# Kernel tuning notes

Hardware: AMD Instinct MI355X
Metric: run time of the kernel (lower is better)

Reference implementation:

```python
import math
import jax, jax.numpy as jnp
import numpy as np

B, S, H = 8, 2048, 1024
NH = 1
DH = H // NH          # head dim == hidden since NH=1 (required by module's math)
DT = 64               # distance_type


def setup_inputs() -> dict:
    key = jax.random.key(0)
    ks = jax.random.split(key, 10)
    hidden_states = jax.random.normal(ks[0], (B, S, H), dtype=jnp.float32)
    attention_mask = jnp.zeros((B, 1, 1, S), dtype=jnp.float32)
    word_word_relation = jax.random.randint(ks[1], (B, S, S), 0, DT, dtype=jnp.int32)
    init = 0.02
    Wq = jax.random.normal(ks[2], (H, H), dtype=jnp.float32) * init
    bq = jnp.zeros((H,), dtype=jnp.float32)
    Wk = jax.random.normal(ks[3], (H, H), dtype=jnp.float32) * init
    bk = jnp.zeros((H,), dtype=jnp.float32)
    Wv = jax.random.normal(ks[4], (H, H), dtype=jnp.float32) * init
    bv = jnp.zeros((H,), dtype=jnp.float32)
    dist_emb = jax.random.normal(ks[5], (DT, H), dtype=jnp.float32) * init
    dist_emb = dist_emb.at[0].set(0.0)  # padding_idx=0
    return {
        "hidden_states": hidden_states,
        "attention_mask": attention_mask,
        "word_word_relation": word_word_relation,
        "Wq": Wq, "bq": bq, "Wk": Wk, "bk": bk, "Wv": Wv, "bv": bv,
        "dist_emb": dist_emb,
    }


def reference(hidden_states, attention_mask, word_word_relation,
              Wq, bq, Wk, bk, Wv, bv, dist_emb):
    b, s, h = hidden_states.shape
    def heads(x):  # [b,s,h] -> [b,nh,s,dh]
        return x.reshape(b, s, NH, DH).transpose(0, 2, 1, 3)
    q = heads(hidden_states @ Wq.T + bq)
    k = heads(hidden_states @ Wk.T + bk)
    v = heads(hidden_states @ Wv.T + bv)

    scores = jnp.einsum('bhqd,bhkd->bhqk', q, k)                 # [b,nh,s,s]
    word_dot_distance = jnp.einsum('bhqd,td->bhqt', q, dist_emb) # [b,nh,s,DT]

    idx = word_word_relation[:, None, :, :]                      # [b,1,s,s]
    bias = jnp.take_along_axis(word_dot_distance, idx, axis=3)
    mask_out = (word_word_relation == 1)[:, None].astype(scores.dtype)
    bias = bias * mask_out

    scores = (scores + bias) / math.sqrt(DH) + attention_mask
    probs = jax.nn.softmax(scores, axis=-1)
    ctx = jnp.einsum('bhqk,bhkd->bhqd', probs, v)
    ctx = ctx.transpose(0, 2, 1, 3).reshape(b, s, h)
    return ctx
```

## Files before the change

### kernel.cpp

```cpp
#include <hip/hip_runtime.h>

typedef unsigned short u16;
typedef __bf16 bf16x8 __attribute__((ext_vector_type(8)));
typedef u16 u16x8 __attribute__((ext_vector_type(8)));
typedef float f32x4 __attribute__((ext_vector_type(4)));

#define S_LEN 2048
#define H_LEN 1024

__device__ __forceinline__ u16 f2b(float f) {
  unsigned u = __float_as_uint(f);
  return (u16)((u + 0x7FFFu + ((u >> 16) & 1u)) >> 16);
}
__device__ __forceinline__ float b2f(u16 h) { return __uint_as_float(((unsigned)h) << 16); }

#define GLOAD16(gp, lp)                                   \
  __builtin_amdgcn_global_load_lds(                       \
      (__attribute__((address_space(1))) void*)(gp),      \
      (__attribute__((address_space(3))) void*)(lp), 16, 0, 0)

#define FENCE() asm volatile("" ::: "memory")
#define PBAR()                           \
  do {                                   \
    FENCE();                             \
    __builtin_amdgcn_s_barrier();        \
    FENCE();                             \
  } while (0)
#define WAIT_LGKM0()                                        \
  do {                                                      \
    asm volatile("s_waitcnt lgkmcnt(0)" ::: "memory");      \
    __builtin_amdgcn_sched_barrier(0);                      \
  } while (0)
#define WAIT_VM(n) asm volatile("s_waitcnt vmcnt(" #n ")" ::: "memory")

__device__ __forceinline__ f32x4 MM(bf16x8 a, bf16x8 b, f32x4 c) {
  return __builtin_amdgcn_mfma_f32_16x16x32_bf16(a, b, c, 0, 0, 0);
}

__global__ __launch_bounds__(256) void prep_kernel(
    const float* __restrict__ X, const float* __restrict__ Wq,
    const float* __restrict__ Wk, const float* __restrict__ Wv,
    const float* __restrict__ bq, const float* __restrict__ bk,
    const float* __restrict__ bv, const float* __restrict__ dist,
    const int* __restrict__ rel,
    u16* __restrict__ Xbf, u16* __restrict__ Wbf, float* __restrict__ b_all,
    u16* __restrict__ de1, unsigned* __restrict__ bits, float* __restrict__ d1) {
  size_t tid = (size_t)blockIdx.x * blockDim.x + threadIdx.x;
  size_t nth = (size_t)gridDim.x * blockDim.x;
  for (size_t i = tid; i < 4194304u; i += nth) {
    float4 v = ((const float4*)X)[i];
    ushort4 o; o.x = f2b(v.x); o.y = f2b(v.y); o.z = f2b(v.z); o.w = f2b(v.w);
    ((ushort4*)Xbf)[i] = o;
  }
  for (size_t i = tid; i < 786432u; i += nth) {
    int which = (int)(i >> 18);
    size_t off = i & 262143u;
    const float4* src = (const float4*)(which == 0 ? Wq : (which == 1 ? Wk : Wv));
    float4 v = src[off];
    ushort4 o; o.x = f2b(v.x); o.y = f2b(v.y); o.z = f2b(v.z); o.w = f2b(v.w);
    ((ushort4*)Wbf)[i] = o;
  }
  const int4* r4 = (const int4*)rel;
  for (size_t wi = tid; wi < 1048576u; wi += nth) {
    const int4* s = r4 + wi * 8;
    unsigned m = 0;
#pragma unroll
    for (int u = 0; u < 8; ++u) {
      int4 v = s[u];
      m |= (unsigned)(v.x == 1) << (u * 4 + 0);
      m |= (unsigned)(v.y == 1) << (u * 4 + 1);
      m |= (unsigned)(v.z == 1) << (u * 4 + 2);
      m |= (unsigned)(v.w == 1) << (u * 4 + 3);
    }
    bits[wi] = m;
  }
  for (size_t i = tid; i < 256u; i += nth) {
    float4 v = ((const float4*)(dist + H_LEN))[i];
    ushort4 o; o.x = f2b(v.x); o.y = f2b(v.y); o.z = f2b(v.z); o.w = f2b(v.w);
    ((ushort4*)de1)[i] = o;
  }
  for (size_t i = tid; i < 3072u; i += nth)
    b_all[i] = (i < 1024) ? bq[i] : (i < 2048 ? bk[i - 1024] : bv[i - 2048]);
  for (size_t i = tid; i < 32768u; i += nth) d1[i] = 0.f;
}

struct GArgs {
  const u16* A; const u16* B;
  long long sA, sB;
  int ldA, ldB, K;
  u16 *Qo, *Ko, *Vo; const float* b_all; const u16* de1; float* d1;
  const unsigned* relbits; const float* mask; u16* P; float* denom;
  float* outp;
};

template <int EPI>
__global__ __launch_bounds__(512, 2) void gemm256(GArgs g) {
  int bx, by, bz;
  {
    const int lin = blockIdx.x;
    if constexpr (EPI == 0) {
      const int wg = (lin & 7) * 96 + (lin >> 3);
      by = wg / 12; bx = wg % 12; bz = 0;
    } else if constexpr (EPI == 1) {
      const int wg = (lin & 7) * 64 + (lin >> 3);
      bz = wg >> 6; by = (wg >> 3) & 7; bx = wg & 7;
    } else {
      const int wg = (lin & 7) * 32 + (lin >> 3);
      bz = wg >> 5; by = (wg >> 2) & 7; bx = wg & 3;
    }
  }
  const u16* Abase = g.A + (size_t)bz * g.sA;
  const u16* Bbase = g.B + (size_t)bz * g.sB;
  const int m0 = by * 256, n0 = bx * 256;

  __shared__ u16 smem[65536];

  const int tid = threadIdx.x;
  const int lane = tid & 63, w = tid >> 6;
  const int wm = w >> 2, wn = w & 3;
  const int l15 = lane & 15, quad = lane >> 4;

  f32x4 acc[8][4];
  const f32x4 zero = {0.f, 0.f, 0.f, 0.f};
#pragma unroll
  for (int a = 0; a < 8; ++a)
#pragma unroll
    for (int b = 0; b < 4; ++b) acc[a][b] = zero;

  const u16* gA[4]; const u16* gB[4]; int qoff[4];
#pragma unroll
  for (int r = 0; r < 4; ++r) {
    const int q = r * 512 + tid;
    const int row = q >> 3, ch = q & 7;
    const int chS = ch ^ (row & 7);
    gA[r] = Abase + (size_t)(m0 + row) * g.ldA + chS * 8;
    gB[r] = Bbase + (size_t)(n0 + row) * g.ldB + chS * 8;
    qoff[r] = q * 8;
  }

  const int NT = g.K >> 6;

  auto stage2 = [&](int tile, int pr) {
    if (tile >= NT) return;
    const int boff2 = (tile & 1) << 15;
    const int kt = tile << 6;
    if (pr < 2) {
      GLOAD16(gA[2 * pr] + kt,     &smem[boff2 + qoff[2 * pr]]);
      GLOAD16(gA[2 * pr + 1] + kt, &smem[boff2 + qoff[2 * pr + 1]]);
    } else {
      const int r = 2 * (pr - 2);
      GLOAD16(gB[r] + kt,     &smem[boff2 + 16384 + qoff[r]]);
      GLOAD16(gB[r + 1] + kt, &smem[boff2 + 16384 + qoff[r + 1]]);
    }
  };

  stage2(0, 0); stage2(0, 1); stage2(0, 2); stage2(0, 3);
  stage2(1, 0);
  if (1 < NT) { WAIT_VM(2); } else { WAIT_VM(0); }
  PBAR();

  bf16x8 af0[4][2], af1[4][2], bf0[2][2], bf1[2][2];

  for (int t = 0; t < NT; ++t) {
    const int boff = (t & 1) << 15;
    const u16* Ab = smem + boff;
    const u16* Bb = smem + boff + 16384;

#pragma unroll
    for (int mt = 0; mt < 4; ++mt) {
      const int row = wm * 128 + mt * 16 + l15;
      const int base = row * 64, rx = row & 7;
      af0[mt][0] = *(const bf16x8*)&Ab[base + ((quad ^ rx) << 3)];
      af0[mt][1] = *(const bf16x8*)&Ab[base + (((quad + 4) ^ rx) << 3)];
    }
#pragma unroll
    for (int nt = 0; nt < 2; ++nt) {
      const int row = wn * 64 + nt * 16 + l15;
      const int base = row * 64, rx = row & 7;
      bf0[nt][0] = *(const bf16x8*)&Bb[base + ((quad ^ rx) << 3)];
      bf0[nt][1] = *(const bf16x8*)&Bb[base + (((quad + 4) ^ rx) << 3)];
    }
    stage2(t + 1, 1);
    asm volatile("s_waitcnt lgkmcnt(8)" ::: "memory");
    PBAR();
    WAIT_LGKM0();
    __builtin_amdgcn_s_setprio(1);
#pragma unroll
    for (int mt = 0; mt < 4; ++mt)
#pragma unroll
      for (int nt = 0; nt < 2; ++nt) {
        acc[mt][nt] = MM(af0[mt][0], bf0[nt][0], acc[mt][nt]);
        acc[mt][nt] = MM(af0[mt][1], bf0[nt][1], acc[mt][nt]);
      }
    __builtin_amdgcn_s_setprio(0);
    PBAR();

#pragma unroll
    for (int nt = 0; nt < 2; ++nt) {
      const int row = wn * 64 + (nt + 2) * 16 + l15;
      const int base = row * 64, rx = row & 7;
      bf1[nt][0] = *(const bf16x8*)&Bb[base + ((quad ^ rx) << 3)];
      bf1[nt][1] = *(const bf16x8*)&Bb[base + (((quad + 4) ^ rx) << 3)];
    }
    stage2(t + 1, 2);
    PBAR();
    WAIT_LGKM0();
    __builtin_amdgcn_s_setprio(1);
#pragma unroll
    for (int mt = 0; mt < 4; ++mt)
#pragma unroll
      for (int nt = 0; nt < 2; ++nt) {
        acc[mt][nt + 2] = MM(af0[mt][0], bf1[nt][0], acc[mt][nt + 2]);
        acc[mt][nt + 2] = MM(af0[mt][1], bf1[nt][1], acc[mt][nt + 2]);
      }
    __builtin_amdgcn_s_setprio(0);
    PBAR();

#pragma unroll
    for (int mt = 0; mt < 4; ++mt) {
      const int row = wm * 128 + (mt + 4) * 16 + l15;
      const int base = row * 64, rx = row & 7;
      af1[mt][0] = *(const bf16x8*)&Ab[base + ((quad ^ rx) << 3)];
      af1[mt][1] = *(const bf16x8*)&Ab[base + (((quad + 4) ^ rx) << 3)];
    }
    stage2(t + 1, 3);
    PBAR();
    WAIT_LGKM0();
    __builtin_amdgcn_s_setprio(1);
#pragma unroll
    for (int mt = 0; mt < 4; ++mt)
#pragma unroll
      for (int nt = 0; nt < 2; ++nt) {
        acc[mt + 4][nt] = MM(af1[mt][0], bf0[nt][0], acc[mt + 4][nt]);
        acc[mt + 4][nt] = MM(af1[mt][1], bf0[nt][1], acc[mt + 4][nt]);
      }
    __builtin_amdgcn_s_setprio(0);
    PBAR();

    stage2(t + 2, 0);
    PBAR();
    WAIT_LGKM0();
    __builtin_amdgcn_s_setprio(1);
#pragma unroll
    for (int mt = 0; mt < 4; ++mt)
#pragma unroll
      for (int nt = 0; nt < 2; ++nt) {
        acc[mt + 4][nt + 2] = MM(af1[mt][0], bf1[nt][0], acc[mt + 4][nt + 2]);
        acc[mt + 4][nt + 2] = MM(af1[mt][1], bf1[nt][1], acc[mt + 4][nt + 2]);
      }
    __builtin_amdgcn_s_setprio(0);
    if (t + 2 < NT) {
      WAIT_VM(2);
    } else if (t + 1 < NT) {
      WAIT_VM(0);
    }
    PBAR();
  }

  const int nbase = n0 + wn * 64;

  if constexpr (EPI == 0) {
    const int which = n0 >> 10;
    const int nl0 = n0 & 1023;
    float bv4[4], dw[4];
#pragma unroll
    for (int nt = 0; nt < 4; ++nt) {
      const int col = wn * 64 + nt * 16 + l15;
      bv4[nt] = g.b_all[n0 + col];
      dw[nt] = (which == 0) ? b2f(g.de1[nl0 + col]) : 0.f;
    }
#pragma unroll
    for (int mt = 0; mt < 8; ++mt)
#pragma unroll
      for (int r = 0; r < 4; ++r) {
        const int row = wm * 128 + mt * 16 + quad * 4 + r;
        float part = 0.f;
#pragma unroll
        for (int nt = 0; nt < 4; ++nt) {
          const float v = acc[mt][nt][r] + bv4[nt];
          part += v * dw[nt];
          const int col = wn * 64 + nt * 16 + l15;
          const int chS = (col >> 3) ^ (row & 31);
          smem[row * 256 + chS * 8 + (col & 7)] = f2b(v);
        }
        if (which == 0) {
          part += __shfl_xor(part, 1);
          part += __shfl_xor(part, 2);
          part += __shfl_xor(part, 4);
          part += __shfl_xor(part, 8);
          if (l15 == 0) atomicAdd(&g.d1[m0 + row], part);
        }
      }
    __syncthreads();
    u16* dstbuf = which == 0 ? g.Qo : (which == 1 ? g.Ko : g.Vo);
#pragma unroll
    for (int p = 0; p < 16; ++p) {
      const int flat = p * 512 + tid;
      const int row = flat >> 5, chunk = flat & 31;
      const int chS = chunk ^ (row & 31);
      u16x8 v = *(const u16x8*)&smem[row * 256 + chS * 8];
      *(u16x8*)(dstbuf + (size_t)(m0 + row) * H_LEN + nl0 + chunk * 8) = v;
    }
  }

  if constexpr (EPI == 1) {
    float mk[4];
#pragma unroll
    for (int nt = 0; nt < 4; ++nt) mk[nt] = g.mask[bz * S_LEN + nbase + nt * 16 + l15];
    const size_t bSS = (size_t)bz * S_LEN * S_LEN;
    const int wbase = (n0 + wn * 64) >> 5;
#pragma unroll
    for (int mt = 0; mt < 8; ++mt)
#pragma unroll
      for (int r = 0; r < 4; ++r) {
        const int row = wm * 128 + mt * 16 + quad * 4 + r;
        const int gi = bz * S_LEN + m0 + row;
        const float d1v = g.d1[gi] * 0.03125f;
        const unsigned w0 = g.relbits[(size_t)gi * 64 + wbase];
        const unsigned w1 = g.relbits[(size_t)gi * 64 + wbase + 1];
        float dsum = 0.f;
#pragma unroll
        for (int nt = 0; nt < 4; ++nt) {
          const unsigned word = (nt & 2) ? w1 : w0;
          const int pos = (nt * 16 + l15) & 31;
          const float bias = ((word >> pos) & 1) ? d1v : 0.f;
          const float logit = acc[mt][nt][r] * 0.03125f + bias + mk[nt];
          const float pv = __expf(logit);
          const u16 pb = f2b(pv);
          dsum += b2f(pb);
          const int col = wn * 64 + nt * 16 + l15;
          const int chS = (col >> 3) ^ (row & 31);
          smem[row * 256 + chS * 8 + (col & 7)] = pb;
        }
        dsum += __shfl_xor(dsum, 1);
        dsum += __shfl_xor(dsum, 2);
        dsum += __shfl_xor(dsum, 4);
        dsum += __shfl_xor(dsum, 8);
        if (l15 == 0) atomicAdd(&g.denom[gi], dsum);
      }
    __syncthreads();
#pragma unroll
    for (int p = 0; p < 16; ++p) {
      const int flat = p * 512 + tid;
      const int row = flat >> 5, chunk = flat & 31;
      const int chS = chunk ^ (row & 31);
      u16x8 v = *(const u16x8*)&smem[row * 256 + chS * 8];
      *(u16x8*)(g.P + bSS + (size_t)(m0 + row) * S_LEN + n0 + chunk * 8) = v;
    }
  }

  if constexpr (EPI == 2) {
    const size_t ob = (size_t)bz * S_LEN * H_LEN;
#pragma unroll
    for (int mt = 0; mt < 8; ++mt)
#pragma unroll
      for (int r = 0; r < 4; ++r) {
        const int row = wm * 128 + mt * 16 + quad * 4 + r;
        const float inv = 1.0f / g.denom[bz * S_LEN + m0 + row];
        const size_t rowo = ob + (size_t)(m0 + row) * H_LEN;
#pragma unroll
        for (int nt = 0; nt < 4; ++nt)
          g.outp[rowo + nbase + nt * 16 + l15] = acc[mt][nt][r] * inv;
      }
  }
}

__global__ __launch_bounds__(256) void transpose_v(const u16* __restrict__ V,
                                                   u16* __restrict__ Vt) {
  const int b = blockIdx.z;
  const int j0 = blockIdx.x * 64;
  const int d0 = blockIdx.y * 64;
  __shared__ u16 t[64][72];
  const int tid = threadIdx.x;
  const int tr = tid >> 4;
  const int tc = (tid & 15) * 4;
#pragma unroll
  for (int p = 0; p < 4; ++p) {
    const int jl = p * 16 + tr;
    const u16* src = V + ((size_t)b * S_LEN + (j0 + jl)) * H_LEN + d0 + tc;
    ushort4 v = *(const ushort4*)src;
    t[jl][tc + 0] = v.x; t[jl][tc + 1] = v.y; t[jl][tc + 2] = v.z; t[jl][tc + 3] = v.w;
  }
  __syncthreads();
#pragma unroll
  for (int p = 0; p < 4; ++p) {
    const int dl = p * 16 + tr;
    ushort4 v;
    v.x = t[tc + 0][dl]; v.y = t[tc + 1][dl]; v.z = t[tc + 2][dl]; v.w = t[tc + 3][dl];
    *(ushort4*)(Vt + ((size_t)b * H_LEN + (d0 + dl)) * S_LEN + j0 + tc) = v;
  }
}

extern "C" void kernel_launch(void* const* d_in, const int* in_sizes, int n_in,
                              void* d_out, int out_size, void* d_ws, size_t ws_size,
                              hipStream_t stream) {
  (void)in_sizes; (void)n_in; (void)out_size; (void)ws_size;
  const float* X    = (const float*)d_in[0];
  const float* mask = (const float*)d_in[1];
  const int*   rel  = (const int*)d_in[2];
  const float* Wq   = (const float*)d_in[3];
  const float* bq   = (const float*)d_in[4];
  const float* Wk   = (const float*)d_in[5];
  const float* bk   = (const float*)d_in[6];
  const float* Wv   = (const float*)d_in[7];
  const float* bv   = (const float*)d_in[8];
  const float* dist = (const float*)d_in[9];
  float* out = (float*)d_out;

  char* p = (char*)d_ws;
  u16* Xbf = (u16*)p;      p += (size_t)16384 * 1024 * 2;
  u16* Wbf = (u16*)p;      p += (size_t)3072 * 1024 * 2;
  float* b_all = (float*)p; p += 3072 * 4;
  u16* de1 = (u16*)p;      p += 4096;
  u16* Qb = (u16*)p;       p += (size_t)16384 * 1024 * 2;
  u16* Kb = (u16*)p;       p += (size_t)16384 * 1024 * 2;
  u16* Vb = (u16*)p;       p += (size_t)16384 * 1024 * 2;
  u16* Vt = (u16*)p;       p += (size_t)16384 * 1024 * 2;
  float* d1 = (float*)p;   p += 16384 * 4;
  float* denom = (float*)p; p += 16384 * 4;
  unsigned* relbits = (unsigned*)p; p += (size_t)1048576 * 4;
  u16* P = (u16*)p;        p += (size_t)8 * 2048 * 2048 * 2;

  prep_kernel<<<1024, 256, 0, stream>>>(X, Wq, Wk, Wv, bq, bk, bv, dist, rel,
                                        Xbf, Wbf, b_all, de1, relbits, d1);

  GArgs g0 = {};
  g0.A = Xbf; g0.B = Wbf; g0.sA = 0; g0.sB = 0;
  g0.ldA = 1024; g0.ldB = 1024; g0.K = 1024;
  g0.Qo = Qb; g0.Ko = Kb; g0.Vo = Vb; g0.b_all = b_all; g0.de1 = de1; g0.d1 = d1;
  gemm256<0><<<dim3(768, 1, 1), dim3(512, 1, 1), 0, stream>>>(g0);

  transpose_v<<<dim3(32, 16, 8), dim3(256, 1, 1), 0, stream>>>(Vb, Vt);

  GArgs g1 = {};
  g1.A = Qb; g1.B = Kb; g1.sA = 2048LL * 1024; g1.sB = 2048LL * 1024;
  g1.ldA = 1024; g1.ldB = 1024; g1.K = 1024;
  g1.relbits = relbits; g1.d1 = d1; g1.mask = mask; g1.P = P; g1.denom = denom;
  gemm256<1><<<dim3(512, 1, 1), dim3(512, 1, 1), 0, stream>>>(g1);

  GArgs g2 = {};
  g2.A = P; g2.B = Vt; g2.sA = 2048LL * 2048; g2.sB = 1024LL * 2048;
  g2.ldA = 2048; g2.ldB = 2048; g2.K = 2048;
  g2.denom = denom; g2.outp = out;
  gemm256<2><<<dim3(256, 1, 1), dim3(512, 1, 1), 0, stream>>>(g2);
}
```

Measured before the change: 594.0 us.

## Fuse V transpose into projection epilogue, restage GEMM loads, coalesce relation bitpacking

The V projection epilogue now writes V already transposed through shared memory, so the separate transpose kernel and the intermediate V buffer are removed. The QKV and QK^T GEMMs switch from staggered partial-tile staging to issuing a full tile's loads two tiles ahead with deeper vmcnt waits. The QK^T block index mapping drops the XCD-swizzled order for a plain linear order. The relation-mask bitpacking now has each thread read one contiguous int4 and assemble 32-bit masks with lane shuffles, giving coalesced loads.

```diff
diff --git a/kernel.cpp b/kernel.cpp
--- a/kernel.cpp
+++ b/kernel.cpp
@@ -47,6 +47,7 @@
     u16* __restrict__ de1, unsigned* __restrict__ bits, float* __restrict__ d1) {
   size_t tid = (size_t)blockIdx.x * blockDim.x + threadIdx.x;
   size_t nth = (size_t)gridDim.x * blockDim.x;
+  const int lane = threadIdx.x & 63;
   for (size_t i = tid; i < 4194304u; i += nth) {
     float4 v = ((const float4*)X)[i];
     ushort4 o; o.x = f2b(v.x); o.y = f2b(v.y); o.z = f2b(v.z); o.w = f2b(v.w);
@@ -61,18 +62,17 @@
     ((ushort4*)Wbf)[i] = o;
   }
   const int4* r4 = (const int4*)rel;
-  for (size_t wi = tid; wi < 1048576u; wi += nth) {
-    const int4* s = r4 + wi * 8;
-    unsigned m = 0;
-#pragma unroll
-    for (int u = 0; u < 8; ++u) {
-      int4 v = s[u];
-      m |= (unsigned)(v.x == 1) << (u * 4 + 0);
-      m |= (unsigned)(v.y == 1) << (u * 4 + 1);
-      m |= (unsigned)(v.z == 1) << (u * 4 + 2);
-      m |= (unsigned)(v.w == 1) << (u * 4 + 3);
-    }
-    bits[wi] = m;
+  for (size_t c = tid; c < 8388608u; c += nth) {
+    int4 v = r4[c];
+    unsigned nib = (unsigned)(v.x == 1) | ((unsigned)(v.y == 1) << 1) |
+                   ((unsigned)(v.z == 1) << 2) | ((unsigned)(v.w == 1) << 3);
+    unsigned o1 = __shfl_xor((int)nib, 1);
+    nib = (lane & 1) ? (o1 | (nib << 4)) : (nib | (o1 << 4));
+    unsigned o2 = __shfl_xor((int)nib, 2);
+    nib = (lane & 2) ? (o2 | (nib << 8)) : (nib | (o2 << 8));
+    unsigned o4 = __shfl_xor((int)nib, 4);
+    nib = (lane & 4) ? (o4 | (nib << 16)) : (nib | (o4 << 16));
+    if ((lane & 7) == 0) bits[c >> 3] = nib;
   }
   for (size_t i = tid; i < 256u; i += nth) {
     float4 v = ((const float4*)(dist + H_LEN))[i];
@@ -88,7 +88,7 @@
   const u16* A; const u16* B;
   long long sA, sB;
   int ldA, ldB, K;
-  u16 *Qo, *Ko, *Vo; const float* b_all; const u16* de1; float* d1;
+  u16 *Qo, *Ko, *Vt; const float* b_all; const u16* de1; float* d1;
   const unsigned* relbits; const float* mask; u16* P; float* denom;
   float* outp;
 };
@@ -102,8 +102,7 @@
       const int wg = (lin & 7) * 96 + (lin >> 3);
       by = wg / 12; bx = wg % 12; bz = 0;
     } else if constexpr (EPI == 1) {
-      const int wg = (lin & 7) * 64 + (lin >> 3);
-      bz = wg >> 6; by = (wg >> 3) & 7; bx = wg & 7;
+      bx = lin & 7; by = (lin >> 3) & 7; bz = lin >> 6;
     } else {
       const int wg = (lin & 7) * 32 + (lin >> 3);
       bz = wg >> 5; by = (wg >> 2) & 7; bx = wg & 3;
@@ -140,6 +139,12 @@
 
   const int NT = g.K >> 6;
 
+  auto stageFull = [&](int boff2, int kt) {
+#pragma unroll
+    for (int r = 0; r < 4; ++r) GLOAD16(gA[r] + kt, &smem[boff2 + qoff[r]]);
+#pragma unroll
+    for (int r = 0; r < 4; ++r) GLOAD16(gB[r] + kt, &smem[boff2 + 16384 + qoff[r]]);
+  };
   auto stage2 = [&](int tile, int pr) {
     if (tile >= NT) return;
     const int boff2 = (tile & 1) << 15;
@@ -154,107 +159,207 @@
     }
   };
 
-  stage2(0, 0); stage2(0, 1); stage2(0, 2); stage2(0, 3);
-  stage2(1, 0);
-  if (1 < NT) { WAIT_VM(2); } else { WAIT_VM(0); }
-  PBAR();
-
   bf16x8 af0[4][2], af1[4][2], bf0[2][2], bf1[2][2];
 
-  for (int t = 0; t < NT; ++t) {
-    const int boff = (t & 1) << 15;
-    const u16* Ab = smem + boff;
-    const u16* Bb = smem + boff + 16384;
-
-#pragma unroll
-    for (int mt = 0; mt < 4; ++mt) {
-      const int row = wm * 128 + mt * 16 + l15;
-      const int base = row * 64, rx = row & 7;
-      af0[mt][0] = *(const bf16x8*)&Ab[base + ((quad ^ rx) << 3)];
-      af0[mt][1] = *(const bf16x8*)&Ab[base + (((quad + 4) ^ rx) << 3)];
-    }
-#pragma unroll
-    for (int nt = 0; nt < 2; ++nt) {
-      const int row = wn * 64 + nt * 16 + l15;
-      const int base = row * 64, rx = row & 7;
-      bf0[nt][0] = *(const bf16x8*)&Bb[base + ((quad ^ rx) << 3)];
-      bf0[nt][1] = *(const bf16x8*)&Bb[base + (((quad + 4) ^ rx) << 3)];
-    }
-    stage2(t + 1, 1);
-    asm volatile("s_waitcnt lgkmcnt(8)" ::: "memory");
+  if constexpr (EPI != 2) {
+    stageFull(0, 0);
+    if (1 < NT) stageFull(32768, 64);
+    WAIT_VM(8);
     PBAR();
-    WAIT_LGKM0();
-    __builtin_amdgcn_s_setprio(1);
-#pragma unroll
-    for (int mt = 0; mt < 4; ++mt)
+
+    for (int t = 0; t < NT; ++t) {
+      const int boff = (t & 1) << 15;
+      const u16* Ab = smem + boff;
+      const u16* Bb = smem + boff + 16384;
+
+#pragma unroll
+      for (int mt = 0; mt < 4; ++mt) {
+        const int row = wm * 128 + mt * 16 + l15;
+        const int base = row * 64, rx = row & 7;
+        af0[mt][0] = *(const bf16x8*)&Ab[base + ((quad ^ rx) << 3)];
+        af0[mt][1] = *(const bf16x8*)&Ab[base + (((quad + 4) ^ rx) << 3)];
+      }
 #pragma unroll
       for (int nt = 0; nt < 2; ++nt) {
-        acc[mt][nt] = MM(af0[mt][0], bf0[nt][0], acc[mt][nt]);
-        acc[mt][nt] = MM(af0[mt][1], bf0[nt][1], acc[mt][nt]);
-      }
-    __builtin_amdgcn_s_setprio(0);
+        const int row = wn * 64 + nt * 16 + l15;
+        const int base = row * 64, rx = row & 7;
+        bf0[nt][0] = *(const bf16x8*)&Bb[base + ((quad ^ rx) << 3)];
+        bf0[nt][1] = *(const bf16x8*)&Bb[base + (((quad + 4) ^ rx) << 3)];
+      }
+      asm volatile("s_waitcnt lgkmcnt(8)" ::: "memory");
+      PBAR();
+      WAIT_LGKM0();
+      __builtin_amdgcn_s_setprio(1);
+#pragma unroll
+      for (int mt = 0; mt < 4; ++mt)
+#pragma unroll
+        for (int nt = 0; nt < 2; ++nt) {
+          acc[mt][nt] = MM(af0[mt][0], bf0[nt][0], acc[mt][nt]);
+          acc[mt][nt] = MM(af0[mt][1], bf0[nt][1], acc[mt][nt]);
+        }
+      __builtin_amdgcn_s_setprio(0);
+      PBAR();
+
+#pragma unroll
+      for (int nt = 0; nt < 2; ++nt) {
+        const int row = wn * 64 + (nt + 2) * 16 + l15;
+        const int base = row * 64, rx = row & 7;
+        bf1[nt][0] = *(const bf16x8*)&Bb[base + ((quad ^ rx) << 3)];
+        bf1[nt][1] = *(const bf16x8*)&Bb[base + (((quad + 4) ^ rx) << 3)];
+      }
+      PBAR();
+      WAIT_LGKM0();
+      __builtin_amdgcn_s_setprio(1);
+#pragma unroll
+      for (int mt = 0; mt < 4; ++mt)
+#pragma unroll
+        for (int nt = 0; nt < 2; ++nt) {
+          acc[mt][nt + 2] = MM(af0[mt][0], bf1[nt][0], acc[mt][nt + 2]);
+          acc[mt][nt + 2] = MM(af0[mt][1], bf1[nt][1], acc[mt][nt + 2]);
+        }
+      __builtin_amdgcn_s_setprio(0);
+      PBAR();
+
+#pragma unroll
+      for (int mt = 0; mt < 4; ++mt) {
+        const int row = wm * 128 + (mt + 4) * 16 + l15;
+        const int base = row * 64, rx = row & 7;
+        af1[mt][0] = *(const bf16x8*)&Ab[base + ((quad ^ rx) << 3)];
+        af1[mt][1] = *(const bf16x8*)&Ab[base + (((quad + 4) ^ rx) << 3)];
+      }
+      PBAR();
+      WAIT_LGKM0();
+      __builtin_amdgcn_s_setprio(1);
+#pragma unroll
+      for (int mt = 0; mt < 4; ++mt)
+#pragma unroll
+        for (int nt = 0; nt < 2; ++nt) {
+          acc[mt + 4][nt] = MM(af1[mt][0], bf0[nt][0], acc[mt + 4][nt]);
+          acc[mt + 4][nt] = MM(af1[mt][1], bf0[nt][1], acc[mt + 4][nt]);
+        }
+      __builtin_amdgcn_s_setprio(0);
+      PBAR();
+
+      if (t + 2 < NT) stageFull(boff, (t + 2) << 6);
+      PBAR();
+      WAIT_LGKM0();
+      __builtin_amdgcn_s_setprio(1);
+#pragma unroll
+      for (int mt = 0; mt < 4; ++mt)
+#pragma unroll
+        for (int nt = 0; nt < 2; ++nt) {
+          acc[mt + 4][nt + 2] = MM(af1[mt][0], bf1[nt][0], acc[mt + 4][nt + 2]);
+          acc[mt + 4][nt + 2] = MM(af1[mt][1], bf1[nt][1], acc[mt + 4][nt + 2]);
+        }
+      __builtin_amdgcn_s_setprio(0);
+      if (t + 2 < NT) {
+        WAIT_VM(8);
+      } else if (t + 1 < NT) {
+        WAIT_VM(0);
+      }
+      PBAR();
+    }
+  } else {
+    stage2(0, 0); stage2(0, 1); stage2(0, 2); stage2(0, 3);
+    stage2(1, 0);
+    if (1 < NT) { WAIT_VM(2); } else { WAIT_VM(0); }
     PBAR();
 
-#pragma unroll
-    for (int nt = 0; nt < 2; ++nt) {
-      const int row = wn * 64 + (nt + 2) * 16 + l15;
-      const int base = row * 64, rx = row & 7;
-      bf1[nt][0] = *(const bf16x8*)&Bb[base + ((quad ^ rx) << 3)];
-      bf1[nt][1] = *(const bf16x8*)&Bb[base + (((quad + 4) ^ rx) << 3)];
-    }
-    stage2(t + 1, 2);
-    PBAR();
-    WAIT_LGKM0();
-    __builtin_amdgcn_s_setprio(1);
-#pragma unroll
-    for (int mt = 0; mt < 4; ++mt)
+    for (int t = 0; t < NT; ++t) {
+      const int boff = (t & 1) << 15;
+      const u16* Ab = smem + boff;
+      const u16* Bb = smem + boff + 16384;
+
+#pragma unroll
+      for (int mt = 0; mt < 4; ++mt) {
+        const int row = wm * 128 + mt * 16 + l15;
+        const int base = row * 64, rx = row & 7;
+        af0[mt][0] = *(const bf16x8*)&Ab[base + ((quad ^ rx) << 3)];
+        af0[mt][1] = *(const bf16x8*)&Ab[base + (((quad + 4) ^ rx) << 3)];
+      }
 #pragma unroll
       for (int nt = 0; nt < 2; ++nt) {
-        acc[mt][nt + 2] = MM(af0[mt][0], bf1[nt][0], acc[mt][nt + 2]);
-        acc[mt][nt + 2] = MM(af0[mt][1], bf1[nt][1], acc[mt][nt + 2]);
-      }
-    __builtin_amdgcn_s_setprio(0);
-    PBAR();
-
-#pragma unroll
-    for (int mt = 0; mt < 4; ++mt) {
-      const int row = wm * 128 + (mt + 4) * 16 + l15;
-      const int base = row * 64, rx = row & 7;
-      af1[mt][0] = *(const bf16x8*)&Ab[base + ((quad ^ rx) << 3)];
-      af1[mt][1] = *(const bf16x8*)&Ab[base + (((quad + 4) ^ rx) << 3)];
-    }
-    stage2(t + 1, 3);
-    PBAR();
-    WAIT_LGKM0();
-    __builtin_amdgcn_s_setprio(1);
-#pragma unroll
-    for (int mt = 0; mt < 4; ++mt)
+        const int row = wn * 64 + nt * 16 + l15;
+        const int base = row * 64, rx = row & 7;
+        bf0[nt][0] = *(const bf16x8*)&Bb[base + ((quad ^ rx) << 3)];
+        bf0[nt][1] = *(const bf16x8*)&Bb[base + (((quad + 4) ^ rx) << 3)];
+      }
+      stage2(t + 1, 1);
+      asm volatile("s_waitcnt lgkmcnt(8)" ::: "memory");
+      PBAR();
+      WAIT_LGKM0();
+      __builtin_amdgcn_s_setprio(1);
+#pragma unroll
+      for (int mt = 0; mt < 4; ++mt)
+#pragma unroll
+        for (int nt = 0; nt < 2; ++nt) {
+          acc[mt][nt] = MM(af0[mt][0], bf0[nt][0], acc[mt][nt]);
+          acc[mt][nt] = MM(af0[mt][1], bf0[nt][1], acc[mt][nt]);
+        }
+      __builtin_amdgcn_s_setprio(0);
+      PBAR();
+
 #pragma unroll
       for (int nt = 0; nt < 2; ++nt) {
-        acc[mt + 4][nt] = MM(af1[mt][0], bf0[nt][0], acc[mt + 4][nt]);
-        acc[mt + 4][nt] = MM(af1[mt][1], bf0[nt][1], acc[mt + 4][nt]);
-      }
-    __builtin_amdgcn_s_setprio(0);
-    PBAR();
-
-    stage2(t + 2, 0);
-    PBAR();
-    WAIT_LGKM0();
-    __builtin_amdgcn_s_setprio(1);
-#pragma unroll
-    for (int mt = 0; mt < 4; ++mt)
-#pragma unroll
-      for (int nt = 0; nt < 2; ++nt) {
-        acc[mt + 4][nt + 2] = MM(af1[mt][0], bf1[nt][0], acc[mt + 4][nt + 2]);
-        acc[mt + 4][nt + 2] = MM(af1[mt][1], bf1[nt][1], acc[mt + 4][nt + 2]);
-      }
-    __builtin_amdgcn_s_setprio(0);
-    if (t + 2 < NT) {
-      WAIT_VM(2);
-    } else if (t + 1 < NT) {
-      WAIT_VM(0);
-    }
-    PBAR();
+        const int row = wn * 64 + (nt + 2) * 16 + l15;
+        const int base = row * 64, rx = row & 7;
+        bf1[nt][0] = *(const bf16x8*)&Bb[base + ((quad ^ rx) << 3)];
+        bf1[nt][1] = *(const bf16x8*)&Bb[base + (((quad + 4) ^ rx) << 3)];
+      }
+      stage2(t + 1, 2);
+      PBAR();
+      WAIT_LGKM0();
+      __builtin_amdgcn_s_setprio(1);
+#pragma unroll
+      for (int mt = 0; mt < 4; ++mt)
+#pragma unroll
+        for (int nt = 0; nt < 2; ++nt) {
+          acc[mt][nt + 2] = MM(af0[mt][0], bf1[nt][0], acc[mt][nt + 2]);
+          acc[mt][nt + 2] = MM(af0[mt][1], bf1[nt][1], acc[mt][nt + 2]);
+        }
+      __builtin_amdgcn_s_setprio(0);
+      PBAR();
+
+#pragma unroll
+      for (int mt = 0; mt < 4; ++mt) {
+        const int row = wm * 128 + (mt + 4) * 16 + l15;
+        const int base = row * 64, rx = row & 7;
+        af1[mt][0] = *(const bf16x8*)&Ab[base + ((quad ^ rx) << 3)];
+        af1[mt][1] = *(const bf16x8*)&Ab[base + (((quad + 4) ^ rx) << 3)];
+      }
+      stage2(t + 1, 3);
+      PBAR();
+      WAIT_LGKM0();
+      __builtin_amdgcn_s_setprio(1);
+#pragma unroll
+      for (int mt = 0; mt < 4; ++mt)
+#pragma unroll
+        for (int nt = 0; nt < 2; ++nt) {
+          acc[mt + 4][nt] = MM(af1[mt][0], bf0[nt][0], acc[mt + 4][nt]);
+          acc[mt + 4][nt] = MM(af1[mt][1], bf0[nt][1], acc[mt + 4][nt]);
+        }
+      __builtin_amdgcn_s_setprio(0);
+      PBAR();
+
+      stage2(t + 2, 0);
+      PBAR();
+      WAIT_LGKM0();
+      __builtin_amdgcn_s_setprio(1);
+#pragma unroll
+      for (int mt = 0; mt < 4; ++mt)
+#pragma unroll
+        for (int nt = 0; nt < 2; ++nt) {
+          acc[mt + 4][nt + 2] = MM(af1[mt][0], bf1[nt][0], acc[mt + 4][nt + 2]);
+          acc[mt + 4][nt + 2] = MM(af1[mt][1], bf1[nt][1], acc[mt + 4][nt + 2]);
+        }
+      __builtin_amdgcn_s_setprio(0);
+      if (t + 2 < NT) {
+        WAIT_VM(2);
+      } else if (t + 1 < NT) {
+        WAIT_VM(0);
+      }
+      PBAR();
+    }
   }
 
   const int nbase = n0 + wn * 64;
@@ -269,37 +374,64 @@
       bv4[nt] = g.b_all[n0 + col];
       dw[nt] = (which == 0) ? b2f(g.de1[nl0 + col]) : 0.f;
     }
-#pragma unroll
-    for (int mt = 0; mt < 8; ++mt)
-#pragma unroll
-      for (int r = 0; r < 4; ++r) {
-        const int row = wm * 128 + mt * 16 + quad * 4 + r;
-        float part = 0.f;
-#pragma unroll
-        for (int nt = 0; nt < 4; ++nt) {
-          const float v = acc[mt][nt][r] + bv4[nt];
-          part += v * dw[nt];
-          const int col = wn * 64 + nt * 16 + l15;
-          const int chS = (col >> 3) ^ (row & 31);
-          smem[row * 256 + chS * 8 + (col & 7)] = f2b(v);
-        }
-        if (which == 0) {
-          part += __shfl_xor(part, 1);
-          part += __shfl_xor(part, 2);
-          part += __shfl_xor(part, 4);
-          part += __shfl_xor(part, 8);
-          if (l15 == 0) atomicAdd(&g.d1[m0 + row], part);
-        }
-      }
-    __syncthreads();
-    u16* dstbuf = which == 0 ? g.Qo : (which == 1 ? g.Ko : g.Vo);
-#pragma unroll
-    for (int p = 0; p < 16; ++p) {
-      const int flat = p * 512 + tid;
-      const int row = flat >> 5, chunk = flat & 31;
-      const int chS = chunk ^ (row & 31);
-      u16x8 v = *(const u16x8*)&smem[row * 256 + chS * 8];
-      *(u16x8*)(dstbuf + (size_t)(m0 + row) * H_LEN + nl0 + chunk * 8) = v;
+    if (which < 2) {
+#pragma unroll
+      for (int mt = 0; mt < 8; ++mt)
+#pragma unroll
+        for (int r = 0; r < 4; ++r) {
+          const int row = wm * 128 + mt * 16 + quad * 4 + r;
+          float part = 0.f;
+#pragma unroll
+          for (int nt = 0; nt < 4; ++nt) {
+            const float v = acc[mt][nt][r] + bv4[nt];
+            part += v * dw[nt];
+            const int col = wn * 64 + nt * 16 + l15;
+            const int chS = (col >> 3) ^ (row & 31);
+            smem[row * 256 + chS * 8 + (col & 7)] = f2b(v);
+          }
+          if (which == 0) {
+            part += __shfl_xor(part, 1);
+            part += __shfl_xor(part, 2);
+            part += __shfl_xor(part, 4);
+            part += __shfl_xor(part, 8);
+            if (l15 == 0) atomicAdd(&g.d1[m0 + row], part);
+          }
+        }
+      __syncthreads();
+      u16* dstbuf = which == 0 ? g.Qo : g.Ko;
+#pragma unroll
+      for (int p = 0; p < 16; ++p) {
+        const int flat = p * 512 + tid;
+        const int row = flat >> 5, chunk = flat & 31;
+        const int chS = chunk ^ (row & 31);
+        u16x8 v = *(const u16x8*)&smem[row * 256 + chS * 8];
+        *(u16x8*)(dstbuf + (size_t)(m0 + row) * H_LEN + nl0 + chunk * 8) = v;
+      }
+    } else {
+#pragma unroll
+      for (int mt = 0; mt < 8; ++mt)
+#pragma unroll
+        for (int r = 0; r < 4; ++r) {
+          const int row = wm * 128 + mt * 16 + quad * 4 + r;
+#pragma unroll
+          for (int nt = 0; nt < 4; ++nt) {
+            const float v = acc[mt][nt][r] + bv4[nt];
+            const int col = wn * 64 + nt * 16 + l15;
+            const int chS = (row >> 3) ^ (col & 31);
+            smem[col * 256 + chS * 8 + (row & 7)] = f2b(v);
+          }
+        }
+      __syncthreads();
+      const int batch = m0 >> 11, sl0 = m0 & 2047;
+#pragma unroll
+      for (int p = 0; p < 16; ++p) {
+        const int flat = p * 512 + tid;
+        const int dimc = flat >> 5, chunk = flat & 31;
+        const int chS = chunk ^ (dimc & 31);
+        u16x8 v = *(const u16x8*)&smem[dimc * 256 + chS * 8];
+        *(u16x8*)(g.Vt + ((size_t)batch * H_LEN + nl0 + dimc) * S_LEN + sl0 +
+                  chunk * 8) = v;
+      }
     }
   }
 
@@ -362,32 +494,6 @@
         for (int nt = 0; nt < 4; ++nt)
           g.outp[rowo + nbase + nt * 16 + l15] = acc[mt][nt][r] * inv;
       }
-  }
-}
-
-__global__ __launch_bounds__(256) void transpose_v(const u16* __restrict__ V,
-                                                   u16* __restrict__ Vt) {
-  const int b = blockIdx.z;
-  const int j0 = blockIdx.x * 64;
-  const int d0 = blockIdx.y * 64;
-  __shared__ u16 t[64][72];
-  const int tid = threadIdx.x;
-  const int tr = tid >> 4;
-  const int tc = (tid & 15) * 4;
-#pragma unroll
-  for (int p = 0; p < 4; ++p) {
-    const int jl = p * 16 + tr;
-    const u16* src = V + ((size_t)b * S_LEN + (j0 + jl)) * H_LEN + d0 + tc;
-    ushort4 v = *(const ushort4*)src;
-    t[jl][tc + 0] = v.x; t[jl][tc + 1] = v.y; t[jl][tc + 2] = v.z; t[jl][tc + 3] = v.w;
-  }
-  __syncthreads();
-#pragma unroll
-  for (int p = 0; p < 4; ++p) {
-    const int dl = p * 16 + tr;
-    ushort4 v;
-    v.x = t[tc + 0][dl]; v.y = t[tc + 1][dl]; v.z = t[tc + 2][dl]; v.w = t[tc + 3][dl];
-    *(ushort4*)(Vt + ((size_t)b * H_LEN + (d0 + dl)) * S_LEN + j0 + tc) = v;
   }
 }
 
@@ -414,7 +520,6 @@
   u16* de1 = (u16*)p;      p += 4096;
   u16* Qb = (u16*)p;       p += (size_t)16384 * 1024 * 2;
   u16* Kb = (u16*)p;       p += (size_t)16384 * 1024 * 2;
-  u16* Vb = (u16*)p;       p += (size_t)16384 * 1024 * 2;
   u16* Vt = (u16*)p;       p += (size_t)16384 * 1024 * 2;
   float* d1 = (float*)p;   p += 16384 * 4;
   float* denom = (float*)p; p += 16384 * 4;
@@ -427,10 +532,8 @@
   GArgs g0 = {};
   g0.A = Xbf; g0.B = Wbf; g0.sA = 0; g0.sB = 0;
   g0.ldA = 1024; g0.ldB = 1024; g0.K = 1024;
-  g0.Qo = Qb; g0.Ko = Kb; g0.Vo = Vb; g0.b_all = b_all; g0.de1 = de1; g0.d1 = d1;
+  g0.Qo = Qb; g0.Ko = Kb; g0.Vt = Vt; g0.b_all = b_all; g0.de1 = de1; g0.d1 = d1;
   gemm256<0><<<dim3(768, 1, 1), dim3(512, 1, 1), 0, stream>>>(g0);
-
-  transpose_v<<<dim3(32, 16, 8), dim3(256, 1, 1), 0, stream>>>(Vb, Vt);
 
   GArgs g1 = {};
   g1.A = Qb; g1.B = Kb; g1.sA = 2048LL * 1024; g1.sB = 2048LL * 1024;
```

New measurement: 570.0 us. 1.04x faster.
